# Optimization experiments

Measured on AMD Instinct MI355X. Metric: run time of the kernel, lower is better.

Reference implementation:

```python
import jax, jax.numpy as jnp
import numpy as np

KH, KW = 5, 5  # kernel; stride=1, padding=0, dilation=1 per init_kwargs


def _unfold(x, kh, kw):
    # torch.nn.functional.unfold with stride=1, pad=0, dil=1, channel-major
    # ordering: out channel index = c*kh*kw + i*kw + j
    B, C, H, W = x.shape
    oh, ow = H - kh + 1, W - kw + 1
    patches = jnp.stack(
        [x[:, :, i:i + oh, j:j + ow] for i in range(kh) for j in range(kw)],
        axis=2,
    )  # [B, C, kh*kw, oh, ow]
    return patches.reshape(B, C * kh * kw, oh, ow)


def _sample_spikes(inp_conv, T):
    # multinomial(replacement=True) over the Cf channel dim per (b, x, y)
    logits = jnp.log(inp_conv.transpose(0, 2, 3, 1))  # [B, OH, OW, Cf]
    B, OH, OW, _ = logits.shape
    return jax.random.categorical(
        jax.random.key(42), logits[:, None], axis=-1, shape=(B, T, OH, OW)
    )  # [B, T, OH, OW] int


def setup_inputs() -> dict:
    key = jax.random.key(0)
    ks = jax.random.split(key, 6)
    B, C, H, W = 32, 24, 28, 28
    OH, OW = 24, 24
    Hn = 128  # number of hidden neurons
    T = 96    # number of spikes
    Cf = C * KH * KW  # 600
    return {
        "input": jax.random.uniform(ks[0], (B, C, H, W), jnp.float32, 0.01, 1.0),
        "epsilon_xy": jax.random.uniform(ks[1], (OH, OW, KH, KW), jnp.float32, 0.1, 1.0),
        "epsilon_0": jax.random.uniform(ks[2], (1,), jnp.float32, 0.5, 1.0),
        "epsilon_t": jax.random.uniform(ks[3], (T,), jnp.float32, 0.5, 1.0),
        "weights": jax.random.uniform(ks[4], (Cf, Hn), jnp.float32, 0.0, 1.0),
        "h_initial": jax.random.uniform(ks[5], (Hn,), jnp.float32, 0.5, 1.0),
        "number_of_spikes": T,
    }


def reference(input, epsilon_xy, epsilon_0, epsilon_t, weights, h_initial,
              number_of_spikes):
    T = int(number_of_spikes)
    B, C = input.shape[0], input.shape[1]
    inp_conv = _unfold(input, KH, KW)              # [B, Cf, OH, OW]
    spikes = _sample_spikes(inp_conv, T)           # [B, T, OH, OW]
    OH, OW = spikes.shape[2], spikes.shape[3]

    # epsilon_xy_convolved: value independent of input channel c,
    # index c*KH*KW + k -> epsilon_xy[x, y] flat at k. Stored as [OH, OW, Cf].
    eps_conv = jnp.tile(epsilon_xy.reshape(OH, OW, KH * KW), (1, 1, C))
    eps0 = epsilon_0[0]

    # Normalized recurrence: g = h / epsilon_scale (exactly equivalent to the
    # original h/epsilon_scale bookkeeping, including the overflow-rescale branch):
    #   g' = (g + eps_sub * (W[s]*g) / sum(W[s]*g)) / (1 + eps_sub)
    Hn = h_initial.shape[0]
    g0 = jnp.broadcast_to(h_initial, (B, OH, OW, Hn)).astype(jnp.float32)

    def step(g, xs):
        s, et = xs                                  # s: [B, OH, OW]
        wg = weights[s] * g                         # [B, OH, OW, Hn]
        denom = jnp.sum(wg, axis=-1, keepdims=True)  # [B, OH, OW, 1]
        eps = jnp.take_along_axis(eps_conv[None], s[..., None], axis=-1)
        eps_sub = eps * (et * eps0)                 # [B, OH, OW, 1]
        factor = jnp.nan_to_num(eps_sub / denom, nan=0.0, posinf=0.0, neginf=0.0)
        g = (g + wg * factor) / (1.0 + eps_sub)
        return g, None

    g, _ = jax.lax.scan(step, g0, (jnp.moveaxis(spikes, 1, 0), epsilon_t[:T]))
    return jnp.moveaxis(g, 3, 1)                    # [B, Hn, OH, OW]
```

## Files before the change

kernel.cpp:

```cpp
#include <hip/hip_runtime.h>
#include <stdint.h>

constexpr int Bn = 32, Cc = 24, Hh = 28, Ww = 28;
constexpr int OHt = 24, OWt = 24;
constexpr int CF = 600, HN = 128, TT = 96;
constexpr int NPIX = OHt * OWt;
constexpr int NSAMP = Bn * TT * NPIX;
constexpr int NLOG = Bn * Cc * Hh * Ww;

__device__ __forceinline__ uint32_t threefry_0_42_pre(uint32_t x1) {
  const uint32_t ks1 = 42u, ks2 = 0x1BD11BF0u;
  uint32_t x0 = x1;
  x1 = __builtin_rotateleft32(x1, 13) ^ x0;
  x0 += x1; x1 = __builtin_rotateleft32(x1, 15) ^ x0;
  x0 += x1; x1 = __builtin_rotateleft32(x1, 26) ^ x0;
  x0 += x1; x1 = __builtin_rotateleft32(x1,  6) ^ x0;
  x0 += ks1; x1 += ks2 + 1u;
  x0 += x1; x1 = __builtin_rotateleft32(x1, 17) ^ x0;
  x0 += x1; x1 = __builtin_rotateleft32(x1, 29) ^ x0;
  x0 += x1; x1 = __builtin_rotateleft32(x1, 16) ^ x0;
  x0 += x1; x1 = __builtin_rotateleft32(x1, 24) ^ x0;
  x0 += ks2; x1 += 2u;
  x0 += x1; x1 = __builtin_rotateleft32(x1, 13) ^ x0;
  x0 += x1; x1 = __builtin_rotateleft32(x1, 15) ^ x0;
  x0 += x1; x1 = __builtin_rotateleft32(x1, 26) ^ x0;
  x0 += x1; x1 = __builtin_rotateleft32(x1,  6) ^ x0;
  x1 += ks1 + 3u;
  x0 += x1; x1 = __builtin_rotateleft32(x1, 17) ^ x0;
  x0 += x1; x1 = __builtin_rotateleft32(x1, 29) ^ x0;
  x0 += x1; x1 = __builtin_rotateleft32(x1, 16) ^ x0;
  x0 += x1; x1 = __builtin_rotateleft32(x1, 24) ^ x0;
  x0 += ks1; x1 += ks2 + 4u;
  x0 += x1; x1 = __builtin_rotateleft32(x1, 13) ^ x0;
  x0 += x1; x1 = __builtin_rotateleft32(x1, 15) ^ x0;
  x0 += x1; x1 = __builtin_rotateleft32(x1, 26) ^ x0;
  x0 += x1; x1 = __builtin_rotateleft32(x1,  6) ^ x0;
  x0 += ks2; x1 += 5u;
  return x0 ^ x1;
}

__global__ __launch_bounds__(256) void k_rinc(const float* __restrict__ in,
                                              float* __restrict__ rc) {
  int i = blockIdx.x * 256 + threadIdx.x;
  if (i < NLOG) rc[i] = 1.1920928955078125e-7f / in[i];
}

__device__ __attribute__((noinline)) int exact_argmax(
    uint32_t base, const float* __restrict__ inb) {
  float best = -1e30f;
  int bi = 0;
  int cf = 0;
  #pragma unroll 1
  for (int c = 0; c < Cc; ++c) {
    const float* inc = inb + c * (Hh * Ww);
    #pragma unroll 1
    for (int ki = 0; ki < 5; ++ki)
      #pragma unroll
      for (int kj = 0; kj < 5; ++kj) {
        uint32_t bits = threefry_0_42_pre(base + (uint32_t)cf);
        uint32_t key = bits >> 9;
        float f = __uint_as_float(key | 0x3f800000u) - 1.0f;
        float u = (f == 0.0f) ? 1.17549435e-38f : f;
        float l1 = logf(u);
        float v = -logf(-l1) + logf(inc[ki * Ww + kj]);
        if (v > best) { best = v; bi = cf; }
        ++cf;
      }
  }
  return bi;
}

__global__ __launch_bounds__(256) void k_sample(const float* __restrict__ rincp,
                                                const float* __restrict__ input,
                                                int* __restrict__ spikes) {
  int tid = blockIdx.x * 256 + threadIdx.x;
  int y = tid % OWt;
  int x = (tid / OWt) % OHt;
  int t = (tid / NPIX) % 48;
  int b = tid / (NPIX * 48);
  int sid1 = ((b * TT + t) * OHt + x) * OWt + y;
  uint32_t ctr1 = (uint32_t)sid1 * 600u + 42u;
  const float* rcb = rincp + (b * Cc) * (Hh * Ww) + x * Ww + y;

  uint32_t m1a = 0xFFFFFFFFu, m2a = 0xFFFFFFFFu;
  uint32_t m1b = 0xFFFFFFFFu, m2b = 0xFFFFFFFFu;

#define SURR(BITS, RC, M1, M2)                                              \
  {                                                                         \
    uint32_t key = (BITS) >> 9;                                             \
    float tailf = (float)(0x800000u - key);             \
    float s = (RC)*tailf;                                       \
    float T = tailf * 1.1920928955078125e-7f;             \
    float q = __builtin_fmaf(                                               \
        T, __builtin_fmaf(T, 0.33333333333f, 0.5f), 1.0f);                  \
    float rh = s * q;                                                       \
    uint32_t pk = (__float_as_uint(rh) & 0xFFFFFC00u) | (uint32_t)cf;       \
    uint32_t tmp = (pk > M1) ? pk : M1;                            \
    M2 = (M2 < tmp) ? M2 : tmp;                                    \
    M1 = (M1 < pk) ? M1 : pk;                                      \
  }

  int cf = 0;
  #pragma unroll 1
  for (int c = 0; c < Cc; ++c) {
    const float* rcc = rcb + c * (Hh * Ww);
    #pragma unroll
    for (int ki = 0; ki < 5; ++ki) {
      #pragma unroll
      for (int kj = 0; kj < 5; ++kj) {
        float rc = rcc[ki * Ww + kj];
        uint32_t c1 = ctr1 + (uint32_t)cf;
        uint32_t bb1 = threefry_0_42_pre(c1);
        uint32_t bb2 = threefry_0_42_pre(c1 + 16588800u);
        SURR(bb1, rc, m1a, m2a)
        SURR(bb2, rc, m1b, m2b)
        ++cf;
      }
    }
  }
#undef SURR

  const float* inb = input + (b * Cc) * (Hh * Ww) + x * Ww + y;
  float f1a = __uint_as_float(m1a & 0xFFFFFC00u);
  float f2a = __uint_as_float(m2a & 0xFFFFFC00u);
  float f1b = __uint_as_float(m1b & 0xFFFFFC00u);
  float f2b = __uint_as_float(m2b & 0xFFFFFC00u);
  constexpr float MARG = 1.0f + 0.0009765625f;
  bool ca = (f1a <= 0.04f) && (f2a > f1a * MARG);
  bool cb = (f1b <= 0.04f) && (f2b > f1b * MARG);
  spikes[sid1] = ca ? (int)(m1a & 1023u) : exact_argmax(ctr1, inb);
  spikes[sid1 + 48 * NPIX] =
      cb ? (int)(m1b & 1023u) : exact_argmax(ctr1 + 16588800u, inb);
}

__global__ __launch_bounds__(256) void k_recur(
    const int* __restrict__ spikes, const float* __restrict__ weights,
    const float* __restrict__ eps_xy, const float* __restrict__ eps_t,
    const float* __restrict__ eps0p, const float* __restrict__ h_init,
    float* __restrict__ out) {
  int wid = blockIdx.x * 4 + (threadIdx.x >> 6);
  int lane = threadIdx.x & 63;
  int y = wid % OWt;
  int x = (wid / OWt) % OHt;
  int b = wid / NPIX;
  float g0 = h_init[lane];
  float g1 = h_init[lane + 64];
  float e0 = eps0p[0];
  const int* sp = spikes + (b * TT) * NPIX + x * OWt + y;
  const float* ex = eps_xy + (x * OWt + y) * 25;
  for (int t = 0; t < TT; ++t) {
    int s = sp[t * NPIX];
    const float* wr = weights + s * HN;
    float wg0 = wr[lane] * g0;
    float wg1 = wr[lane + 64] * g1;
    float sum = wg0 + wg1;
    #pragma unroll
    for (int off = 32; off > 0; off >>= 1) sum += __shfl_xor(sum, off, 64);
    float es = ex[s % 25] * (eps_t[t] * e0);
    float factor = es / sum;
    if (!__builtin_isfinite(factor)) factor = 0.0f;
    float d = 1.0f + es;
    g0 = (g0 + wg0 * factor) / d;
    g1 = (g1 + wg1 * factor) / d;
  }
  out[((b * HN + lane) * OHt + x) * OWt + y] = g0;
  out[((b * HN + lane + 64) * OHt + x) * OWt + y] = g1;
}

extern "C" void kernel_launch(void* const* d_in, const int* in_sizes, int n_in,
                              void* d_out, int out_size, void* d_ws, size_t ws_size,
                              hipStream_t stream) {
  const float* input   = (const float*)d_in[0];
  const float* eps_xy  = (const float*)d_in[1];
  const float* eps0    = (const float*)d_in[2];
  const float* eps_t   = (const float*)d_in[3];
  const float* weights = (const float*)d_in[4];
  const float* h_init  = (const float*)d_in[5];

  float* rinc = (float*)d_ws;
  int* spikes = (int*)((char*)d_ws + NLOG * sizeof(float));

  k_rinc<<<(NLOG + 255) / 256, 256, 0, stream>>>(input, rinc);
  k_sample<<<(NSAMP / 2) / 256, 256, 0, stream>>>(rinc, input, spikes);
  k_recur<<<(Bn * NPIX) / 4, 256, 0, stream>>>(spikes, weights, eps_xy, eps_t,
                                               eps0, h_init, (float*)d_out);
}
```

Measured before the change: 2.896 ms.

## Defer ambiguous samples to a queue resolved by wave-parallel exact argmax kernel

```diff
diff --git a/kernel.cpp b/kernel.cpp
--- a/kernel.cpp
+++ b/kernel.cpp
@@ -7,6 +7,8 @@
 constexpr int NPIX = OHt * OWt;
 constexpr int NSAMP = Bn * TT * NPIX;
 constexpr int NLOG = Bn * Cc * Hh * Ww;
+constexpr int QCAP = 16384;
+constexpr int NOUT = Bn * HN * NPIX;
 
 __device__ __forceinline__ uint32_t threefry_0_42_pre(uint32_t x1) {
   const uint32_t ks1 = 42u, ks2 = 0x1BD11BF0u;
@@ -40,12 +42,22 @@
 }
 
 __global__ __launch_bounds__(256) void k_rinc(const float* __restrict__ in,
-                                              float* __restrict__ rc) {
+                                              float* __restrict__ rc,
+                                              int* __restrict__ qcount) {
   int i = blockIdx.x * 256 + threadIdx.x;
+  if (i == 0) *qcount = 0;
   if (i < NLOG) rc[i] = 1.1920928955078125e-7f / in[i];
 }
 
-__device__ __attribute__((noinline)) int exact_argmax(
+__device__ __forceinline__ float exact_v(uint32_t bits, float lp) {
+  uint32_t key = bits >> 9;
+  float f = __uint_as_float(key | 0x3f800000u) - 1.0f;
+  float u = (f == 0.0f) ? 1.17549435e-38f : f;
+  float l1 = logf(u);
+  return -logf(-l1) + lp;
+}
+
+__device__ __attribute__((noinline)) int exact_argmax_serial(
     uint32_t base, const float* __restrict__ inb) {
   float best = -1e30f;
   int bi = 0;
@@ -57,12 +69,8 @@
     for (int ki = 0; ki < 5; ++ki)
       #pragma unroll
       for (int kj = 0; kj < 5; ++kj) {
-        uint32_t bits = threefry_0_42_pre(base + (uint32_t)cf);
-        uint32_t key = bits >> 9;
-        float f = __uint_as_float(key | 0x3f800000u) - 1.0f;
-        float u = (f == 0.0f) ? 1.17549435e-38f : f;
-        float l1 = logf(u);
-        float v = -logf(-l1) + logf(inc[ki * Ww + kj]);
+        float v = exact_v(threefry_0_42_pre(base + (uint32_t)cf),
+                          logf(inc[ki * Ww + kj]));
         if (v > best) { best = v; bi = cf; }
         ++cf;
       }
@@ -70,9 +78,10 @@
   return bi;
 }
 
-__global__ __launch_bounds__(256) void k_sample(const float* __restrict__ rincp,
-                                                const float* __restrict__ input,
-                                                int* __restrict__ spikes) {
+__global__ __launch_bounds__(256, 8) void k_sample(
+    const float* __restrict__ rincp, const float* __restrict__ input,
+    int* __restrict__ spikes, int* __restrict__ qcount,
+    int* __restrict__ queue) {
   int tid = blockIdx.x * 256 + threadIdx.x;
   int y = tid % OWt;
   int x = (tid / OWt) % OHt;
@@ -88,7 +97,7 @@
 #define SURR(BITS, RC, M1, M2)                                              \
   {                                                                         \
     uint32_t key = (BITS) >> 9;                                             \
-    float tailf = (float)(0x800000u - key);             \
+    float tailf = (float)(0x800000u - key);         \
     float s = (RC)*tailf;                                       \
     float T = tailf * 1.1920928955078125e-7f;             \
     float q = __builtin_fmaf(                                               \
@@ -120,7 +129,6 @@
   }
 #undef SURR
 
-  const float* inb = input + (b * Cc) * (Hh * Ww) + x * Ww + y;
   float f1a = __uint_as_float(m1a & 0xFFFFFC00u);
   float f2a = __uint_as_float(m2a & 0xFFFFFC00u);
   float f1b = __uint_as_float(m1b & 0xFFFFFC00u);
@@ -128,9 +136,60 @@
   constexpr float MARG = 1.0f + 0.0009765625f;
   bool ca = (f1a <= 0.04f) && (f2a > f1a * MARG);
   bool cb = (f1b <= 0.04f) && (f2b > f1b * MARG);
-  spikes[sid1] = ca ? (int)(m1a & 1023u) : exact_argmax(ctr1, inb);
-  spikes[sid1 + 48 * NPIX] =
-      cb ? (int)(m1b & 1023u) : exact_argmax(ctr1 + 16588800u, inb);
+  int sid2 = sid1 + 48 * NPIX;
+  if (ca) {
+    spikes[sid1] = (int)(m1a & 1023u);
+  } else {
+    int qi = atomicAdd(qcount, 1);
+    if (qi < QCAP) queue[qi] = sid1;
+    else spikes[sid1] = exact_argmax_serial(
+             ctr1, input + (b * Cc) * (Hh * Ww) + x * Ww + y);
+  }
+  if (cb) {
+    spikes[sid2] = (int)(m1b & 1023u);
+  } else {
+    int qi = atomicAdd(qcount, 1);
+    if (qi < QCAP) queue[qi] = sid2;
+    else spikes[sid2] = exact_argmax_serial(
+             ctr1 + 16588800u, input + (b * Cc) * (Hh * Ww) + x * Ww + y);
+  }
+}
+
+__global__ __launch_bounds__(256) void k_fix(const int* __restrict__ qcount,
+                                             const int* __restrict__ queue,
+                                             const float* __restrict__ input,
+                                             int* __restrict__ spikes) {
+  int nq = *qcount;
+  if (nq > QCAP) nq = QCAP;
+  int gwid = (blockIdx.x * 256 + threadIdx.x) >> 6;
+  int lane = threadIdx.x & 63;
+  int nwaves = (gridDim.x * 256) >> 6;
+  for (int qi = gwid; qi < nq; qi += nwaves) {
+    int sid = queue[qi];
+    int y = sid % OWt;
+    int x = (sid / OWt) % OHt;
+    int b = sid / (NPIX * TT);
+    uint32_t base = (uint32_t)sid * 600u + 42u;
+    const float* inb = input + (b * Cc) * (Hh * Ww) + x * Ww + y;
+    float best = -1e30f;
+    int bcf = 1024;
+    for (int cf = lane; cf < CF; cf += 64) {
+      int c = cf / 25;
+      int r = cf - c * 25;
+      int ki = r / 5;
+      int kj = r - ki * 5;
+      float v = exact_v(threefry_0_42_pre(base + (uint32_t)cf),
+                        logf(inb[c * (Hh * Ww) + ki * Ww + kj]));
+      if (v > best) { best = v; bcf = cf; }
+    }
+    #pragma unroll
+    for (int off = 32; off > 0; off >>= 1) {
+      float vo = __shfl_xor(best, off, 64);
+      int co = __shfl_xor(bcf, off, 64);
+      if (vo > best || (vo == best && co < bcf)) { best = vo; bcf = co; }
+    }
+    if (lane == 0) spikes[sid] = bcf;
+  }
 }
 
 __global__ __launch_bounds__(256) void k_recur(
@@ -179,9 +238,14 @@
 
   float* rinc = (float*)d_ws;
   int* spikes = (int*)((char*)d_ws + NLOG * sizeof(float));
-
-  k_rinc<<<(NLOG + 255) / 256, 256, 0, stream>>>(input, rinc);
-  k_sample<<<(NSAMP / 2) / 256, 256, 0, stream>>>(rinc, input, spikes);
+  int* outi = (int*)d_out;
+  int* qcount = outi + (NOUT - 1);
+  int* queue = outi + (NOUT - 1 - QCAP);
+
+  k_rinc<<<(NLOG + 255) / 256, 256, 0, stream>>>(input, rinc, qcount);
+  k_sample<<<(NSAMP / 2) / 256, 256, 0, stream>>>(rinc, input, spikes, qcount,
+                                                  queue);
+  k_fix<<<256, 256, 0, stream>>>(qcount, queue, input, spikes);
   k_recur<<<(Bn * NPIX) / 4, 256, 0, stream>>>(spikes, weights, eps_xy, eps_t,
                                                eps0, h_init, (float*)d_out);
 }
```

After: 2.323 ms. 19.8% less time.
